# Performance work log

Measured on AMD Instinct MI355X. Metric: run time of the kernel, lower is better.

Reference implementation:

```python
import jax, jax.numpy as jnp
import numpy as np

N = 10000        # nodes
E = 320000       # edges (avg degree 32)
K = 3            # TAGConv default hops
D_IN, D_H, D_OUT = 256, 128, 64


def setup_inputs() -> dict:
    key = jax.random.key(0)
    ks = jax.random.split(key, 12)
    def w(k, shape):
        # xavier-uniform-ish init
        fan_in, fan_out = shape[-2], shape[-1]
        lim = float(np.sqrt(6.0 / (fan_in + fan_out)))
        return jax.random.uniform(k, shape, jnp.float32, -lim, lim)
    return {
        "x": jax.random.normal(ks[0], (N, D_IN), dtype=jnp.float32),
        "edge_index": jax.random.randint(ks[1], (2, E), 0, N, dtype=jnp.int32),
        "W1": w(ks[2], (K + 1, D_IN, D_H)),  "b1": jnp.zeros((D_H,), jnp.float32),
        "W2": w(ks[3], (K + 1, D_H, D_H)),   "b2": jnp.zeros((D_H,), jnp.float32),
        "W3": w(ks[4], (K + 1, D_H, D_OUT)), "b3": jnp.zeros((D_OUT,), jnp.float32),
        "Wf": w(ks[5], (D_OUT, D_OUT)),      "bf": jnp.zeros((D_OUT,), jnp.float32),
        "Wd": w(ks[6], (D_OUT, D_OUT)),
    }


def _gcn_norm(src, dst, n_nodes):
    # TAGConv's gcn_norm without self-loops: D^-1/2 A D^-1/2 edge weights
    deg = jax.ops.segment_sum(jnp.ones(src.shape, jnp.float32), dst,
                              num_segments=n_nodes)
    dis = jnp.where(deg > 0, jax.lax.rsqrt(jnp.maximum(deg, 1.0)), 0.0)
    return dis[src] * dis[dst]  # [E]


def _tagconv(x, src, dst, norm, W, b):
    # out = sum_{k=0..K} (A_hat^k x) @ W[k] + b
    out = x @ W[0]
    h = x
    for k in range(1, W.shape[0]):
        # message = norm_e * h[src_e], aggregated at dst
        h = jax.ops.segment_sum(norm[:, None] * h[src], dst,
                                num_segments=x.shape[0])
        out = out + h @ W[k]
    return out + b


def reference(x, edge_index, W1, b1, W2, b2, W3, b3, Wf, bf, Wd):
    src, dst = edge_index[0], edge_index[1]
    norm = _gcn_norm(src, dst, x.shape[0])
    h = jax.nn.relu(_tagconv(x, src, dst, norm, W1, b1))
    h = jax.nn.relu(_tagconv(h, src, dst, norm, W2, b2))
    h = jax.nn.relu(_tagconv(h, src, dst, norm, W3, b3))
    z = h @ Wf + bf                     # [N, D_OUT]
    adj = (z @ Wd) @ z.T                # [N, N] bilinear decode
    return adj
```

## Files before the change

kernel.cpp:

```cpp
#include <hip/hip_runtime.h>
#include <hip/hip_bf16.h>
#include <cstdint>
#include <cstddef>


typedef __attribute__((ext_vector_type(8)))  short short8;
typedef __attribute__((ext_vector_type(4)))  float f32x4;
typedef __attribute__((ext_vector_type(16))) float f32x16;

static __device__ __forceinline__ ushort f2bf(float f) {
    __hip_bfloat16 h = __float2bfloat16(f);
    return *reinterpret_cast<const ushort*>(&h);
}
static __device__ __forceinline__ float bf2f(ushort u) {
    union { uint i; float f; } v; v.i = ((uint)u) << 16; return v.f;
}


__global__ void count_kernel(const int* __restrict__ dst, int* __restrict__ counts, int E) {
    int e = blockIdx.x * blockDim.x + threadIdx.x;
    if (e < E) atomicAdd(&counts[dst[e]], 1);
}

__global__ void scan_kernel(const int* __restrict__ counts, int* __restrict__ rowstart,
                            float* __restrict__ dis, int n) {
    __shared__ int sums[1024];
    int t = threadIdx.x;
    int chunk = (n + 1023) / 1024;
    int base = t * chunk;
    int s = 0;
    for (int i = 0; i < chunk; ++i) {
        int idx = base + i;
        if (idx < n) s += counts[idx];
    }
    sums[t] = s;
    __syncthreads();
    for (int off = 1; off < 1024; off <<= 1) {
        int v = (t >= off) ? sums[t - off] : 0;
        __syncthreads();
        sums[t] += v;
        __syncthreads();
    }
    int run = sums[t] - s;
    for (int i = 0; i < chunk; ++i) {
        int idx = base + i;
        if (idx < n) {
            rowstart[idx] = run;
            int c = counts[idx];
            dis[idx] = (c > 0) ? rsqrtf((float)c) : 0.f;
            run += c;
        }
    }
    if (t == 1023) rowstart[n] = sums[1023];
}

__global__ void csr_fill_kernel(const int* __restrict__ src, const int* __restrict__ dst,
                                const float* __restrict__ dis, const int* __restrict__ rowstart,
                                int* __restrict__ cursor, int* __restrict__ csr_src,
                                float* __restrict__ csr_w, int E) {
    int e = blockIdx.x * blockDim.x + threadIdx.x;
    if (e < E) {
        int d = dst[e];
        int s = src[e];
        int pos = rowstart[d] + atomicAdd(&cursor[d], 1);
        csr_src[pos] = s;
        csr_w[pos]   = dis[s] * dis[d];
    }
}

static __device__ __forceinline__ void prep_w_elem(const float* W, ushort* Wt,
                                                   int DIN, int DOUT, int i) {
    int hp  = i / (DIN * DOUT);
    int rem = i - hp * DIN * DOUT;
    int d   = rem / DOUT;
    int o   = rem - d * DOUT;
    Wt[(size_t)o * (4 * DIN) + hp * DIN + d] = f2bf(W[i]);
}
static __device__ __forceinline__ void prep_wt_elem(const float* W, ushort* Wt,
                                                    int K, int C, int i) {
    int k = i / C, c = i - k * C;
    Wt[(size_t)c * K + k] = f2bf(W[i]);
}

__global__ void prep_all_kernel(const float* __restrict__ x, ushort* __restrict__ xb, int nx,
                                const float* __restrict__ W1, ushort* __restrict__ Wt1,
                                const float* __restrict__ W2, ushort* __restrict__ Wt2,
                                const float* __restrict__ W3, ushort* __restrict__ Wt3,
                                const float* __restrict__ Wf, ushort* __restrict__ Wfb,
                                const float* __restrict__ Wd, ushort* __restrict__ Wdb) {
    const int n1 = 4 * 256 * 128, n2 = 4 * 128 * 128, n3 = 4 * 128 * 64, nf = 64 * 64;
    int i = blockIdx.x * blockDim.x + threadIdx.x;
    if (i < nx) { xb[i] = f2bf(x[i]); return; }
    i -= nx;
    if (i < n1) { prep_w_elem(W1, Wt1, 256, 128, i); return; }
    i -= n1;
    if (i < n2) { prep_w_elem(W2, Wt2, 128, 128, i); return; }
    i -= n2;
    if (i < n3) { prep_w_elem(W3, Wt3, 128, 64, i); return; }
    i -= n3;
    if (i < nf) { prep_wt_elem(Wf, Wfb, 64, 64, i); return; }
    i -= nf;
    if (i < nf) { prep_wt_elem(Wd, Wdb, 64, 64, i); return; }
}

template <int D>
__global__ __launch_bounds__(256) void agg4_kernel(
        const ushort* __restrict__ h, const int* __restrict__ rowstart,
        const int* __restrict__ csr_src, const float* __restrict__ csr_w,
        ushort* __restrict__ out, int Nn) {
    constexpr int LPE = D / 8;
    constexpr int EPI = 64 / LPE;
    int wave = threadIdx.x >> 6, lane = threadIdx.x & 63;
    int n = blockIdx.x * 4 + wave;
    if (n >= Nn) return;
    int sub = lane / LPE;
    int ll  = lane % LPE;
    int beg = rowstart[n], end = rowstart[n + 1];

    float acc[8];
    #pragma unroll
    for (int v = 0; v < 8; ++v) acc[v] = 0.f;

    for (int j0 = beg; j0 < end; j0 += 64) {
        int take = end - j0;
        if (take > 64) take = 64;
        int s = 0; float w = 0.f;
        if (lane < take) { s = csr_src[j0 + lane]; w = csr_w[j0 + lane]; }
        for (int i = 0; i < take; i += EPI) {
            int e = i + sub;
            float wi = __shfl(w, e);
            int   si = __shfl(s, e);
            short8 hv = *(const short8*)(h + (size_t)si * D + ll * 8);
            #pragma unroll
            for (int v = 0; v < 8; ++v)
                acc[v] = fmaf(wi, bf2f((ushort)hv[v]), acc[v]);
        }
    }
    if (EPI == 4) {
        #pragma unroll
        for (int v = 0; v < 8; ++v) acc[v] += __shfl_xor(acc[v], 16);
    }
    #pragma unroll
    for (int v = 0; v < 8; ++v) acc[v] += __shfl_xor(acc[v], 32);

    if (sub == 0) {
        short8 o;
        #pragma unroll
        for (int v = 0; v < 8; ++v) o[v] = (short)f2bf(acc[v]);
        *(short8*)(out + (size_t)n * D + ll * 8) = o;
    }
}

template <int DIN, int DOUT>
__global__ __launch_bounds__(256) void tag_gemm_kernel(
        const ushort* __restrict__ A0, const ushort* __restrict__ A1,
        const ushort* __restrict__ A2, const ushort* __restrict__ A3,
        const ushort* __restrict__ Wt, const float* __restrict__ bias,
        ushort* __restrict__ outB, int M) {
    constexpr int CW = DOUT / 4;
    constexpr int NJ = CW / 16;
    constexpr int K4 = 4 * DIN;
    int tid = threadIdx.x, wave = tid >> 6, lane = tid & 63;
    int lr = lane & 15, lk = lane >> 4;
    int r0 = blockIdx.x * 32;
    int c0 = wave * CW;
    int ra0 = min(r0 + lr, M - 1);
    int ra1 = min(r0 + 16 + lr, M - 1);

    f32x4 acc[2][NJ];
    #pragma unroll
    for (int mi = 0; mi < 2; ++mi)
        #pragma unroll
        for (int nj = 0; nj < NJ; ++nj)
            acc[mi][nj] = (f32x4){0.f, 0.f, 0.f, 0.f};

    const ushort* As[4] = {A0, A1, A2, A3};
    #pragma unroll
    for (int hp = 0; hp < 4; ++hp) {
        const ushort* a0p = As[hp] + (size_t)ra0 * DIN + lk * 8;
        const ushort* a1p = As[hp] + (size_t)ra1 * DIN + lk * 8;
        #pragma unroll
        for (int kc = 0; kc < DIN; kc += 32) {
            short8 a0 = *(const short8*)(a0p + kc);
            short8 a1 = *(const short8*)(a1p + kc);
            #pragma unroll
            for (int nj = 0; nj < NJ; ++nj) {
                short8 b = *(const short8*)(Wt + (size_t)(c0 + nj * 16 + lr) * K4
                                            + hp * DIN + kc + lk * 8);
                acc[0][nj] = __builtin_amdgcn_mfma_f32_16x16x32_bf16(a0, b, acc[0][nj], 0, 0, 0);
                acc[1][nj] = __builtin_amdgcn_mfma_f32_16x16x32_bf16(a1, b, acc[1][nj], 0, 0, 0);
            }
        }
    }

    #pragma unroll
    for (int nj = 0; nj < NJ; ++nj) {
        int c = c0 + nj * 16 + lr;
        float bv = bias[c];
        #pragma unroll
        for (int mi = 0; mi < 2; ++mi) {
            int rbase = r0 + mi * 16 + lk * 4;
            #pragma unroll
            for (int r = 0; r < 4; ++r) {
                int row = rbase + r;
                if (row < M) {
                    float v = fmaxf(acc[mi][nj][r] + bv, 0.f);
                    outB[(size_t)row * DOUT + c] = f2bf(v);
                }
            }
        }
    }
}

__global__ __launch_bounds__(256) void lin64_dual_kernel(
        const ushort* __restrict__ A, const ushort* __restrict__ Wfb,
        const float* __restrict__ bias, const ushort* __restrict__ Wdb,
        ushort* __restrict__ zz, ushort* __restrict__ zw, int M) {
    __shared__ ushort zl[4][32][72];
    int tid = threadIdx.x, wave = tid >> 6, lane = tid & 63;
    int lr = lane & 15, lk = lane >> 4;
    int r0 = blockIdx.x * 128 + wave * 32;
    int ra0 = min(r0 + lr, M - 1);
    int ra1 = min(r0 + 16 + lr, M - 1);

    short8 a[2][2], b[4][2];
    #pragma unroll
    for (int kc = 0; kc < 2; ++kc) {
        a[0][kc] = *(const short8*)(A + (size_t)ra0 * 64 + kc * 32 + lk * 8);
        a[1][kc] = *(const short8*)(A + (size_t)ra1 * 64 + kc * 32 + lk * 8);
        #pragma unroll
        for (int nj = 0; nj < 4; ++nj)
            b[nj][kc] = *(const short8*)(Wfb + (size_t)(nj * 16 + lr) * 64 + kc * 32 + lk * 8);
    }
    f32x4 acc1[2][4];
    #pragma unroll
    for (int mi = 0; mi < 2; ++mi)
        #pragma unroll
        for (int nj = 0; nj < 4; ++nj) {
            acc1[mi][nj] = (f32x4){0.f, 0.f, 0.f, 0.f};
            acc1[mi][nj] = __builtin_amdgcn_mfma_f32_16x16x32_bf16(a[mi][0], b[nj][0], acc1[mi][nj], 0, 0, 0);
            acc1[mi][nj] = __builtin_amdgcn_mfma_f32_16x16x32_bf16(a[mi][1], b[nj][1], acc1[mi][nj], 0, 0, 0);
        }

    #pragma unroll
    for (int nj = 0; nj < 4; ++nj) {
        int c = nj * 16 + lr;
        float bv = bias[c];
        #pragma unroll
        for (int mi = 0; mi < 2; ++mi) {
            int rloc = mi * 16 + lk * 4;
            #pragma unroll
            for (int r = 0; r < 4; ++r) {
                ushort u = f2bf(acc1[mi][nj][r] + bv);
                zl[wave][rloc + r][c] = u;
                int row = r0 + rloc + r;
                if (row < M) zz[(size_t)row * 64 + c] = u;
            }
        }
    }
    __syncthreads();

    short8 a2[2][2], b2[4][2];
    #pragma unroll
    for (int kc = 0; kc < 2; ++kc) {
        a2[0][kc] = *(const short8*)&zl[wave][lr][kc * 32 + lk * 8];
        a2[1][kc] = *(const short8*)&zl[wave][16 + lr][kc * 32 + lk * 8];
        #pragma unroll
        for (int nj = 0; nj < 4; ++nj)
            b2[nj][kc] = *(const short8*)(Wdb + (size_t)(nj * 16 + lr) * 64 + kc * 32 + lk * 8);
    }
    f32x4 acc2[2][4];
    #pragma unroll
    for (int mi = 0; mi < 2; ++mi)
        #pragma unroll
        for (int nj = 0; nj < 4; ++nj) {
            acc2[mi][nj] = (f32x4){0.f, 0.f, 0.f, 0.f};
            acc2[mi][nj] = __builtin_amdgcn_mfma_f32_16x16x32_bf16(a2[mi][0], b2[nj][0], acc2[mi][nj], 0, 0, 0);
            acc2[mi][nj] = __builtin_amdgcn_mfma_f32_16x16x32_bf16(a2[mi][1], b2[nj][1], acc2[mi][nj], 0, 0, 0);
        }
    #pragma unroll
    for (int nj = 0; nj < 4; ++nj) {
        int c = nj * 16 + lr;
        #pragma unroll
        for (int mi = 0; mi < 2; ++mi) {
            int rbase = r0 + mi * 16 + lk * 4;
            #pragma unroll
            for (int r = 0; r < 4; ++r) {
                int row = rbase + r;
                if (row < M) zw[(size_t)row * 64 + c] = f2bf(acc2[mi][nj][r]);
            }
        }
    }
}

__global__ __launch_bounds__(256) void decode32_kernel(
        const ushort* __restrict__ ZW, const ushort* __restrict__ Z,
        float* __restrict__ out, int Nn) {
    int tid = threadIdx.x, wave = tid >> 6, lane = tid & 63;
    int wr = wave >> 1, wc = wave & 1;
    int row0 = blockIdx.y * 128 + wr * 64;
    int col0 = blockIdx.x * 128 + wc * 64;
    int lr = lane & 31, hi = lane >> 5;

    short8 a[2][4], b[2][4];
    #pragma unroll
    for (int mi = 0; mi < 2; ++mi) {
        int ra = min(row0 + mi * 32 + lr, Nn - 1);
        int rb = min(col0 + mi * 32 + lr, Nn - 1);
        const ushort* pa = ZW + (size_t)ra * 64 + hi * 8;
        const ushort* pb = Z  + (size_t)rb * 64 + hi * 8;
        #pragma unroll
        for (int kc = 0; kc < 4; ++kc) {
            a[mi][kc] = *(const short8*)(pa + kc * 16);
            b[mi][kc] = *(const short8*)(pb + kc * 16);
        }
    }

    f32x16 acc[2][2];
    #pragma unroll
    for (int mi = 0; mi < 2; ++mi)
        #pragma unroll
        for (int nj = 0; nj < 2; ++nj) {
            f32x16 c;
            #pragma unroll
            for (int q = 0; q < 16; ++q) c[q] = 0.f;
            #pragma unroll
            for (int kc = 0; kc < 4; ++kc)
                c = __builtin_amdgcn_mfma_f32_32x32x16_bf16(a[mi][kc], b[nj][kc], c, 0, 0, 0);
            acc[mi][nj] = c;
        }

    bool full = (row0 + 64 <= Nn) && (col0 + 64 <= Nn);
    #pragma unroll
    for (int mi = 0; mi < 2; ++mi)
        #pragma unroll
        for (int nj = 0; nj < 2; ++nj) {
            int cb = col0 + nj * 32 + lr;
            #pragma unroll
            for (int reg = 0; reg < 16; ++reg) {
                int row = row0 + mi * 32 + (reg & 3) + 8 * (reg >> 2) + 4 * hi;
                if (full) {
                    __builtin_nontemporal_store(acc[mi][nj][reg], &out[(size_t)row * Nn + cb]);
                } else {
                    if (row < Nn && cb < Nn)
                        __builtin_nontemporal_store(acc[mi][nj][reg], &out[(size_t)row * Nn + cb]);
                }
            }
        }
}


extern "C" void kernel_launch(void* const* d_in, const int* in_sizes, int n_in,
                              void* d_out, int out_size, void* d_ws, size_t ws_size,
                              hipStream_t stream) {
    const float* x  = (const float*)d_in[0];
    const int*   ei = (const int*)d_in[1];
    const float* W1 = (const float*)d_in[2];
    const float* b1 = (const float*)d_in[3];
    const float* W2 = (const float*)d_in[4];
    const float* b2 = (const float*)d_in[5];
    const float* W3 = (const float*)d_in[6];
    const float* b3 = (const float*)d_in[7];
    const float* Wf = (const float*)d_in[8];
    const float* bf = (const float*)d_in[9];
    const float* Wd = (const float*)d_in[10];

    const int Nn = in_sizes[0] / 256;
    const int E  = in_sizes[1] / 2;
    const int* src = ei;
    const int* dst = ei + E;

    char* p = (char*)d_ws;
    auto alloc = [&](size_t bytes) -> char* {
        char* r = p;
        p += (bytes + 255) & ~(size_t)255;
        return r;
    };
    size_t nslot = ((size_t)Nn * 4 + 255) & ~(size_t)255;
    int*    counts   = (int*)alloc((size_t)Nn * 4);
    int*    cursor   = (int*)alloc((size_t)Nn * 4);
    int*    rowstart = (int*)alloc((size_t)(Nn + 1) * 4);
    float*  dis      = (float*)alloc((size_t)Nn * 4);
    int*    csr_src  = (int*)alloc((size_t)E * 4);
    float*  csr_w    = (float*)alloc((size_t)E * 4);
    ushort* xb       = (ushort*)alloc((size_t)Nn * 256 * 2);
    ushort* h1b      = (ushort*)alloc((size_t)Nn * 256 * 2);
    ushort* h2b      = (ushort*)alloc((size_t)Nn * 256 * 2);
    ushort* h3b      = (ushort*)alloc((size_t)Nn * 256 * 2);
    ushort* out1b    = (ushort*)alloc((size_t)Nn * 128 * 2);
    ushort* out2b    = (ushort*)alloc((size_t)Nn * 128 * 2);
    ushort* out3b    = (ushort*)alloc((size_t)Nn * 64 * 2);
    ushort* zzb      = (ushort*)alloc((size_t)Nn * 64 * 2);
    ushort* zwb      = (ushort*)alloc((size_t)Nn * 64 * 2);
    ushort* Wt1      = (ushort*)alloc((size_t)128 * 1024 * 2);
    ushort* Wt2      = (ushort*)alloc((size_t)128 * 512 * 2);
    ushort* Wt3      = (ushort*)alloc((size_t)64 * 512 * 2);
    ushort* Wfb      = (ushort*)alloc((size_t)64 * 64 * 2);
    ushort* Wdb      = (ushort*)alloc((size_t)64 * 64 * 2);

    hipMemsetAsync(counts, 0, nslot + (size_t)Nn * 4, stream);

    int eb = (E + 255) / 256;
    count_kernel<<<eb, 256, 0, stream>>>(dst, counts, E);
    scan_kernel<<<1, 1024, 0, stream>>>(counts, rowstart, dis, Nn);
    csr_fill_kernel<<<eb, 256, 0, stream>>>(src, dst, dis, rowstart, cursor,
                                            csr_src, csr_w, E);

    int nx = Nn * 256;
    int nprep = nx + 4 * 256 * 128 + 4 * 128 * 128 + 4 * 128 * 64 + 64 * 64 + 64 * 64;
    prep_all_kernel<<<(nprep + 255) / 256, 256, 0, stream>>>(
        x, xb, nx, W1, Wt1, W2, Wt2, W3, Wt3, Wf, Wfb, Wd, Wdb);

    int ab = (Nn + 3) / 4;
    int gb = (Nn + 31) / 32;

    agg4_kernel<256><<<ab, 256, 0, stream>>>(xb,  rowstart, csr_src, csr_w, h1b, Nn);
    agg4_kernel<256><<<ab, 256, 0, stream>>>(h1b, rowstart, csr_src, csr_w, h2b, Nn);
    agg4_kernel<256><<<ab, 256, 0, stream>>>(h2b, rowstart, csr_src, csr_w, h3b, Nn);
    tag_gemm_kernel<256, 128><<<gb, 256, 0, stream>>>(xb, h1b, h2b, h3b, Wt1, b1, out1b, Nn);

    agg4_kernel<128><<<ab, 256, 0, stream>>>(out1b, rowstart, csr_src, csr_w, h1b, Nn);
    agg4_kernel<128><<<ab, 256, 0, stream>>>(h1b,   rowstart, csr_src, csr_w, h2b, Nn);
    agg4_kernel<128><<<ab, 256, 0, stream>>>(h2b,   rowstart, csr_src, csr_w, h3b, Nn);
    tag_gemm_kernel<128, 128><<<gb, 256, 0, stream>>>(out1b, h1b, h2b, h3b, Wt2, b2, out2b, Nn);

    agg4_kernel<128><<<ab, 256, 0, stream>>>(out2b, rowstart, csr_src, csr_w, h1b, Nn);
    agg4_kernel<128><<<ab, 256, 0, stream>>>(h1b,   rowstart, csr_src, csr_w, h2b, Nn);
    agg4_kernel<128><<<ab, 256, 0, stream>>>(h2b,   rowstart, csr_src, csr_w, h3b, Nn);
    tag_gemm_kernel<128, 64><<<gb, 256, 0, stream>>>(out2b, h1b, h2b, h3b, Wt3, b3, out3b, Nn);

    int lb = (Nn + 127) / 128;
    lin64_dual_kernel<<<lb, 256, 0, stream>>>(out3b, Wfb, bf, Wdb, zzb, zwb, Nn);

    int db = (Nn + 127) / 128;
    decode32_kernel<<<dim3(db, db), 256, 0, stream>>>(zwb, zzb, (float*)d_out, Nn);
}
```

Baseline: 359.0 us.

## Project features before propagation using Horner form to shrink aggregation width

TAGConv is rewritten as y_k = X W_k first, then evaluated Horner-style as out = y0 + A(y1 + A(y2 + A y3)). Each sparse aggregation now works on the output width (128 or 64) instead of the input width (256 for layer 1, and 128 rather than 64 for layer 3). The add of the projected term and the ReLU are fused into the last aggregation. This cuts gather bandwidth in the memory-bound SpMM passes. In exchange there is one wider GEMM that writes four projected outputs, plus extra bf16 rounding of intermediates in a different order.

Measured after the change: 332.3 us. 1.08x faster.

```diff
diff --git a/kernel.cpp b/kernel.cpp
--- a/kernel.cpp
+++ b/kernel.cpp
@@ -68,13 +68,13 @@
     }
 }
 
-static __device__ __forceinline__ void prep_w_elem(const float* W, ushort* Wt,
+static __device__ __forceinline__ void prep_w_elem(const float* W, ushort* Wp,
                                                    int DIN, int DOUT, int i) {
     int hp  = i / (DIN * DOUT);
     int rem = i - hp * DIN * DOUT;
     int d   = rem / DOUT;
     int o   = rem - d * DOUT;
-    Wt[(size_t)o * (4 * DIN) + hp * DIN + d] = f2bf(W[i]);
+    Wp[(size_t)(hp * DOUT + o) * DIN + d] = f2bf(W[i]);
 }
 static __device__ __forceinline__ void prep_wt_elem(const float* W, ushort* Wt,
                                                     int K, int C, int i) {
@@ -83,31 +83,82 @@
 }
 
 __global__ void prep_all_kernel(const float* __restrict__ x, ushort* __restrict__ xb, int nx,
-                                const float* __restrict__ W1, ushort* __restrict__ Wt1,
-                                const float* __restrict__ W2, ushort* __restrict__ Wt2,
-                                const float* __restrict__ W3, ushort* __restrict__ Wt3,
+                                const float* __restrict__ W1, ushort* __restrict__ Wp1,
+                                const float* __restrict__ W2, ushort* __restrict__ Wp2,
+                                const float* __restrict__ W3, ushort* __restrict__ Wp3,
                                 const float* __restrict__ Wf, ushort* __restrict__ Wfb,
                                 const float* __restrict__ Wd, ushort* __restrict__ Wdb) {
     const int n1 = 4 * 256 * 128, n2 = 4 * 128 * 128, n3 = 4 * 128 * 64, nf = 64 * 64;
     int i = blockIdx.x * blockDim.x + threadIdx.x;
     if (i < nx) { xb[i] = f2bf(x[i]); return; }
     i -= nx;
-    if (i < n1) { prep_w_elem(W1, Wt1, 256, 128, i); return; }
+    if (i < n1) { prep_w_elem(W1, Wp1, 256, 128, i); return; }
     i -= n1;
-    if (i < n2) { prep_w_elem(W2, Wt2, 128, 128, i); return; }
+    if (i < n2) { prep_w_elem(W2, Wp2, 128, 128, i); return; }
     i -= n2;
-    if (i < n3) { prep_w_elem(W3, Wt3, 128, 64, i); return; }
+    if (i < n3) { prep_w_elem(W3, Wp3, 128, 64, i); return; }
     i -= n3;
     if (i < nf) { prep_wt_elem(Wf, Wfb, 64, 64, i); return; }
     i -= nf;
     if (i < nf) { prep_wt_elem(Wd, Wdb, 64, 64, i); return; }
 }
 
-template <int D>
-__global__ __launch_bounds__(256) void agg4_kernel(
-        const ushort* __restrict__ h, const int* __restrict__ rowstart,
-        const int* __restrict__ csr_src, const float* __restrict__ csr_w,
-        ushort* __restrict__ out, int Nn) {
+template <int DIN, int DOUT>
+__global__ __launch_bounds__(256) void proj_gemm_kernel(
+        const ushort* __restrict__ A, const ushort* __restrict__ Wp,
+        const float* __restrict__ bias, ushort* __restrict__ y, int M) {
+    constexpr int NJ = DOUT / 16;
+    int tid = threadIdx.x, wave = tid >> 6, lane = tid & 63;
+    int lr = lane & 15, lk = lane >> 4;
+    int r0 = blockIdx.x * 32;
+    int ra0 = min(r0 + lr, M - 1);
+    int ra1 = min(r0 + 16 + lr, M - 1);
+
+    f32x4 acc[2][NJ];
+    #pragma unroll
+    for (int mi = 0; mi < 2; ++mi)
+        #pragma unroll
+        for (int nj = 0; nj < NJ; ++nj)
+            acc[mi][nj] = (f32x4){0.f, 0.f, 0.f, 0.f};
+
+    const ushort* a0p = A + (size_t)ra0 * DIN + lk * 8;
+    const ushort* a1p = A + (size_t)ra1 * DIN + lk * 8;
+    #pragma unroll
+    for (int kc = 0; kc < DIN; kc += 32) {
+        short8 a0 = *(const short8*)(a0p + kc);
+        short8 a1 = *(const short8*)(a1p + kc);
+        #pragma unroll
+        for (int nj = 0; nj < NJ; ++nj) {
+            short8 b = *(const short8*)(Wp + (size_t)(wave * DOUT + nj * 16 + lr) * DIN
+                                        + kc + lk * 8);
+            acc[0][nj] = __builtin_amdgcn_mfma_f32_16x16x32_bf16(a0, b, acc[0][nj], 0, 0, 0);
+            acc[1][nj] = __builtin_amdgcn_mfma_f32_16x16x32_bf16(a1, b, acc[1][nj], 0, 0, 0);
+        }
+    }
+
+    ushort* yw = y + (size_t)wave * M * DOUT;
+    #pragma unroll
+    for (int nj = 0; nj < NJ; ++nj) {
+        int c = nj * 16 + lr;
+        float bv = (wave == 0) ? bias[c] : 0.f;
+        #pragma unroll
+        for (int mi = 0; mi < 2; ++mi) {
+            int rbase = r0 + mi * 16 + lk * 4;
+            #pragma unroll
+            for (int r = 0; r < 4; ++r) {
+                int row = rbase + r;
+                if (row < M)
+                    yw[(size_t)row * DOUT + c] = f2bf(acc[mi][nj][r] + bv);
+            }
+        }
+    }
+}
+
+template <int D, bool RELU>
+__global__ __launch_bounds__(256) void agg5_kernel(
+        const ushort* __restrict__ h, const ushort* __restrict__ yk,
+        const int* __restrict__ rowstart, const int* __restrict__ csr_src,
+        const float* __restrict__ csr_w, ushort* __restrict__ out, int Nn) {
     constexpr int LPE = D / 8;
     constexpr int EPI = 64 / LPE;
     int wave = threadIdx.x >> 6, lane = threadIdx.x & 63;
@@ -136,79 +187,22 @@
                 acc[v] = fmaf(wi, bf2f((ushort)hv[v]), acc[v]);
         }
     }
-    if (EPI == 4) {
-        #pragma unroll
-        for (int v = 0; v < 8; ++v) acc[v] += __shfl_xor(acc[v], 16);
-    }
-    #pragma unroll
-    for (int v = 0; v < 8; ++v) acc[v] += __shfl_xor(acc[v], 32);
+    #pragma unroll
+    for (int off = LPE; off < 64; off <<= 1) {
+        #pragma unroll
+        for (int v = 0; v < 8; ++v) acc[v] += __shfl_xor(acc[v], off);
+    }
 
     if (sub == 0) {
+        short8 yv = *(const short8*)(yk + (size_t)n * D + ll * 8);
         short8 o;
         #pragma unroll
-        for (int v = 0; v < 8; ++v) o[v] = (short)f2bf(acc[v]);
+        for (int v = 0; v < 8; ++v) {
+            float val = acc[v] + bf2f((ushort)yv[v]);
+            if (RELU) val = fmaxf(val, 0.f);
+            o[v] = (short)f2bf(val);
+        }
         *(short8*)(out + (size_t)n * D + ll * 8) = o;
-    }
-}
-
-template <int DIN, int DOUT>
-__global__ __launch_bounds__(256) void tag_gemm_kernel(
-        const ushort* __restrict__ A0, const ushort* __restrict__ A1,
-        const ushort* __restrict__ A2, const ushort* __restrict__ A3,
-        const ushort* __restrict__ Wt, const float* __restrict__ bias,
-        ushort* __restrict__ outB, int M) {
-    constexpr int CW = DOUT / 4;
-    constexpr int NJ = CW / 16;
-    constexpr int K4 = 4 * DIN;
-    int tid = threadIdx.x, wave = tid >> 6, lane = tid & 63;
-    int lr = lane & 15, lk = lane >> 4;
-    int r0 = blockIdx.x * 32;
-    int c0 = wave * CW;
-    int ra0 = min(r0 + lr, M - 1);
-    int ra1 = min(r0 + 16 + lr, M - 1);
-
-    f32x4 acc[2][NJ];
-    #pragma unroll
-    for (int mi = 0; mi < 2; ++mi)
-        #pragma unroll
-        for (int nj = 0; nj < NJ; ++nj)
-            acc[mi][nj] = (f32x4){0.f, 0.f, 0.f, 0.f};
-
-    const ushort* As[4] = {A0, A1, A2, A3};
-    #pragma unroll
-    for (int hp = 0; hp < 4; ++hp) {
-        const ushort* a0p = As[hp] + (size_t)ra0 * DIN + lk * 8;
-        const ushort* a1p = As[hp] + (size_t)ra1 * DIN + lk * 8;
-        #pragma unroll
-        for (int kc = 0; kc < DIN; kc += 32) {
-            short8 a0 = *(const short8*)(a0p + kc);
-            short8 a1 = *(const short8*)(a1p + kc);
-            #pragma unroll
-            for (int nj = 0; nj < NJ; ++nj) {
-                short8 b = *(const short8*)(Wt + (size_t)(c0 + nj * 16 + lr) * K4
-                                            + hp * DIN + kc + lk * 8);
-                acc[0][nj] = __builtin_amdgcn_mfma_f32_16x16x32_bf16(a0, b, acc[0][nj], 0, 0, 0);
-                acc[1][nj] = __builtin_amdgcn_mfma_f32_16x16x32_bf16(a1, b, acc[1][nj], 0, 0, 0);
-            }
-        }
-    }
-
-    #pragma unroll
-    for (int nj = 0; nj < NJ; ++nj) {
-        int c = c0 + nj * 16 + lr;
-        float bv = bias[c];
-        #pragma unroll
-        for (int mi = 0; mi < 2; ++mi) {
-            int rbase = r0 + mi * 16 + lk * 4;
-            #pragma unroll
-            for (int r = 0; r < 4; ++r) {
-                int row = rbase + r;
-                if (row < M) {
-                    float v = fmaxf(acc[mi][nj][r] + bv, 0.f);
-                    outB[(size_t)row * DOUT + c] = f2bf(v);
-                }
-            }
-        }
     }
 }
 
@@ -384,17 +378,17 @@
     int*    csr_src  = (int*)alloc((size_t)E * 4);
     float*  csr_w    = (float*)alloc((size_t)E * 4);
     ushort* xb       = (ushort*)alloc((size_t)Nn * 256 * 2);
-    ushort* h1b      = (ushort*)alloc((size_t)Nn * 256 * 2);
-    ushort* h2b      = (ushort*)alloc((size_t)Nn * 256 * 2);
-    ushort* h3b      = (ushort*)alloc((size_t)Nn * 256 * 2);
+    ushort* yb       = (ushort*)alloc((size_t)4 * Nn * 128 * 2);
+    ushort* t1       = (ushort*)alloc((size_t)Nn * 128 * 2);
+    ushort* t2       = (ushort*)alloc((size_t)Nn * 128 * 2);
     ushort* out1b    = (ushort*)alloc((size_t)Nn * 128 * 2);
     ushort* out2b    = (ushort*)alloc((size_t)Nn * 128 * 2);
     ushort* out3b    = (ushort*)alloc((size_t)Nn * 64 * 2);
     ushort* zzb      = (ushort*)alloc((size_t)Nn * 64 * 2);
     ushort* zwb      = (ushort*)alloc((size_t)Nn * 64 * 2);
-    ushort* Wt1      = (ushort*)alloc((size_t)128 * 1024 * 2);
-    ushort* Wt2      = (ushort*)alloc((size_t)128 * 512 * 2);
-    ushort* Wt3      = (ushort*)alloc((size_t)64 * 512 * 2);
+    ushort* Wp1      = (ushort*)alloc((size_t)512 * 256 * 2);
+    ushort* Wp2      = (ushort*)alloc((size_t)512 * 128 * 2);
+    ushort* Wp3      = (ushort*)alloc((size_t)256 * 128 * 2);
     ushort* Wfb      = (ushort*)alloc((size_t)64 * 64 * 2);
     ushort* Wdb      = (ushort*)alloc((size_t)64 * 64 * 2);
 
@@ -409,25 +403,36 @@
     int nx = Nn * 256;
     int nprep = nx + 4 * 256 * 128 + 4 * 128 * 128 + 4 * 128 * 64 + 64 * 64 + 64 * 64;
     prep_all_kernel<<<(nprep + 255) / 256, 256, 0, stream>>>(
-        x, xb, nx, W1, Wt1, W2, Wt2, W3, Wt3, Wf, Wfb, Wd, Wdb);
+        x, xb, nx, W1, Wp1, W2, Wp2, W3, Wp3, Wf, Wfb, Wd, Wdb);
 
     int ab = (Nn + 3) / 4;
     int gb = (Nn + 31) / 32;
-
-    agg4_kernel<256><<<ab, 256, 0, stream>>>(xb,  rowstart, csr_src, csr_w, h1b, Nn);
-    agg4_kernel<256><<<ab, 256, 0, stream>>>(h1b, rowstart, csr_src, csr_w, h2b, Nn);
-    agg4_kernel<256><<<ab, 256, 0, stream>>>(h2b, rowstart, csr_src, csr_w, h3b, Nn);
-    tag_gemm_kernel<256, 128><<<gb, 256, 0, stream>>>(xb, h1b, h2b, h3b, Wt1, b1, out1b, Nn);
-
-    agg4_kernel<128><<<ab, 256, 0, stream>>>(out1b, rowstart, csr_src, csr_w, h1b, Nn);
-    agg4_kernel<128><<<ab, 256, 0, stream>>>(h1b,   rowstart, csr_src, csr_w, h2b, Nn);
-    agg4_kernel<128><<<ab, 256, 0, stream>>>(h2b,   rowstart, csr_src, csr_w, h3b, Nn);
-    tag_gemm_kernel<128, 128><<<gb, 256, 0, stream>>>(out1b, h1b, h2b, h3b, Wt2, b2, out2b, Nn);
-
-    agg4_kernel<128><<<ab, 256, 0, stream>>>(out2b, rowstart, csr_src, csr_w, h1b, Nn);
-    agg4_kernel<128><<<ab, 256, 0, stream>>>(h1b,   rowstart, csr_src, csr_w, h2b, Nn);
-    agg4_kernel<128><<<ab, 256, 0, stream>>>(h2b,   rowstart, csr_src, csr_w, h3b, Nn);
-    tag_gemm_kernel<128, 64><<<gb, 256, 0, stream>>>(out2b, h1b, h2b, h3b, Wt3, b3, out3b, Nn);
+    size_t Y128 = (size_t)Nn * 128;
+    size_t Y64  = (size_t)Nn * 64;
+
+    proj_gemm_kernel<256, 128><<<gb, 256, 0, stream>>>(xb, Wp1, b1, yb, Nn);
+    agg5_kernel<128, false><<<ab, 256, 0, stream>>>(yb + 3 * Y128, yb + 2 * Y128,
+                                                    rowstart, csr_src, csr_w, t1, Nn);
+    agg5_kernel<128, false><<<ab, 256, 0, stream>>>(t1, yb + 1 * Y128,
+                                                    rowstart, csr_src, csr_w, t2, Nn);
+    agg5_kernel<128, true ><<<ab, 256, 0, stream>>>(t2, yb,
+                                                    rowstart, csr_src, csr_w, out1b, Nn);
+
+    proj_gemm_kernel<128, 128><<<gb, 256, 0, stream>>>(out1b, Wp2, b2, yb, Nn);
+    agg5_kernel<128, false><<<ab, 256, 0, stream>>>(yb + 3 * Y128, yb + 2 * Y128,
+                                                    rowstart, csr_src, csr_w, t1, Nn);
+    agg5_kernel<128, false><<<ab, 256, 0, stream>>>(t1, yb + 1 * Y128,
+                                                    rowstart, csr_src, csr_w, t2, Nn);
+    agg5_kernel<128, true ><<<ab, 256, 0, stream>>>(t2, yb,
+                                                    rowstart, csr_src, csr_w, out2b, Nn);
+
+    proj_gemm_kernel<128, 64><<<gb, 256, 0, stream>>>(out2b, Wp3, b3, yb, Nn);
+    agg5_kernel<64, false><<<ab, 256, 0, stream>>>(yb + 3 * Y64, yb + 2 * Y64,
+                                                   rowstart, csr_src, csr_w, t1, Nn);
+    agg5_kernel<64, false><<<ab, 256, 0, stream>>>(t1, yb + 1 * Y64,
+                                                   rowstart, csr_src, csr_w, t2, Nn);
+    agg5_kernel<64, true ><<<ab, 256, 0, stream>>>(t2, yb,
+                                                   rowstart, csr_src, csr_w, out3b, Nn);
 
     int lb = (Nn + 127) / 128;
     lin64_dual_kernel<<<lb, 256, 0, stream>>>(out3b, Wfb, bf, Wdb, zzb, zwb, Nn);
```
